# Performance work log

Hardware: AMD Instinct MI355X
Metric: run time of the kernel (lower is better)

Reference implementation:

```python
import jax, jax.numpy as jnp
import numpy as np

N = 65536          # total nodes
B = 64             # graphs in batch
NPG = N // B       # nodes per graph (equal-size graphs)
K = 128            # n_clusters (assignment dim)
D_IN = 128         # node feature dim
D = 128            # pooled feature dim
E = 1048576        # edges (avg degree 16)


def setup_inputs() -> dict:
    key = jax.random.key(0)
    k1, k2, k3, k4, k5, k6 = jax.random.split(key, 6)
    h = jax.random.normal(k1, (N, D_IN), dtype=jnp.float32)
    fea = jax.random.normal(k2, (B * K, D), dtype=jnp.float32)
    W_self = jax.random.normal(k3, (D_IN, K), dtype=jnp.float32) / np.sqrt(D_IN)
    W_neigh = jax.random.normal(k4, (D_IN, K), dtype=jnp.float32) / np.sqrt(D_IN)
    b = jnp.zeros((K,), dtype=jnp.float32)
    # edges kept within each graph: sample local ids then offset by graph base
    base = jnp.repeat(jnp.arange(B, dtype=jnp.int64) * NPG, E // B)
    edge_src = jax.random.randint(k5, (E,), 0, NPG, dtype=jnp.int64) + base
    edge_dst = jax.random.randint(k6, (E,), 0, NPG, dtype=jnp.int64) + base
    return {"h": h, "fea": fea, "W_self": W_self, "W_neigh": W_neigh,
            "b": b, "edge_src": edge_src, "edge_dst": edge_dst}


def reference(h, fea, W_self, W_neigh, b, edge_src, edge_dst):
    # GraphSage mean aggregation: neigh[i] = mean_{j: (j->i)} h[j]
    deg = jnp.zeros((N,), h.dtype).at[edge_dst].add(1.0)
    neigh = jnp.zeros((N, D_IN), h.dtype).at[edge_dst].add(h[edge_src])
    neigh = neigh / jnp.maximum(deg, 1.0)[:, None]
    assign = jax.nn.relu(h @ W_self + neigh @ W_neigh + b)       # [N, K]
    assign = jax.nn.softmax(assign, axis=1)                       # softmax over clusters
    # block-diagonal mm == per-graph GEMM: [B, n, K] @ [B, K, D] -> [B, n, D]
    out = jnp.einsum('bnk,bkd->bnd',
                     assign.reshape(B, NPG, K),
                     fea.reshape(B, K, D))
    return out.reshape(N, D)
```

## Files before the change

### kernel.cpp

```cpp
#include <hip/hip_runtime.h>

#define N_NODES 65536
#define B_G     64
#define NPG     1024
#define KC      128
#define DIN     128
#define E_EDGES 1048576
#define EPG     16384
#define NSLICE  8
#define SLICE_E (EPG / NSLICE)
#define CSTRIDE (EPG + NPG)

typedef __attribute__((ext_vector_type(8))) short short8;
typedef __attribute__((ext_vector_type(4))) float floatx4;

static __device__ __forceinline__ short f2bf(float x) {
    unsigned u = __float_as_uint(x);
    unsigned r = (u + 0x7FFF + ((u >> 16) & 1)) >> 16;
    return (short)r;
}
static __device__ __forceinline__ unsigned pack2(float a, float b) {
    return (unsigned)(unsigned short)f2bf(a) | ((unsigned)(unsigned short)f2bf(b) << 16);
}

__global__ __launch_bounds__(256) void setup_a(
    const float* __restrict__ Wself, const float* __restrict__ Wneigh,
    const float* __restrict__ fea, const float* __restrict__ h,
    const int* __restrict__ edst,
    short* __restrict__ wt, short* __restrict__ feaT, short* __restrict__ h_bf,
    int* __restrict__ slicecnt)
{
    int bid = blockIdx.x;
    int tid = threadIdx.x;
    if (bid < B_G * NSLICE) {
        __shared__ int cnt[NPG];
        int g = bid >> 3, s = bid & 7;
        int gbase = g << 10;
        for (int i = tid; i < NPG; i += 256) cnt[i] = 0;
        __syncthreads();
        const int* ed = edst + (size_t)g * EPG + s * SLICE_E;
#pragma unroll
        for (int it = 0; it < SLICE_E / 256; it++)
            atomicAdd(&cnt[ed[it * 256 + tid] - gbase], 1);
        __syncthreads();
        int* sc = slicecnt + ((size_t)bid << 10);
        for (int i = tid; i < NPG; i += 256) sc[i] = cnt[i];
    } else {
        long idx = (long)(bid - B_G * NSLICE) * 256 + tid;
        if (idx < 32768) {
            int n = (int)(idx >> 8), k = (int)(idx & 255);
            float v = (k < 128) ? Wself[k * 128 + n] : Wneigh[(k - 128) * 128 + n];
            wt[idx] = f2bf(v);
        } else if (idx < 32768 + 1048576) {
            long fi = idx - 32768;
            int g = (int)(fi >> 14), d = (int)((fi >> 7) & 127), k = (int)(fi & 127);
            feaT[fi] = f2bf(fea[((long)g * 128 + k) * 128 + d]);
        } else {
            long gi = idx - 32768 - 1048576;
            const float4* hp = (const float4*)h + gi * 2;
            float4 a = hp[0], b4 = hp[1];
            uint4 w;
            w.x = pack2(a.x, a.y);
            w.y = pack2(a.z, a.w);
            w.z = pack2(b4.x, b4.y);
            w.w = pack2(b4.z, b4.w);
            ((uint4*)h_bf)[gi] = w;
        }
    }
}

__global__ __launch_bounds__(1024) void setup_b(
    const int* __restrict__ slicecnt, int* __restrict__ offs,
    int* __restrict__ deg, int* __restrict__ sliceoffs)
{
    __shared__ int sa[NPG];
    int g = blockIdx.x;
    int tid = threadIdx.x;
    int s8[NSLICE];
    int d = 0;
#pragma unroll
    for (int s = 0; s < NSLICE; s++) {
        s8[s] = slicecnt[(((size_t)g * NSLICE + s) << 10) + tid];
        d += s8[s];
    }
    int p = (d + 1) & ~1;
    sa[tid] = p;
    __syncthreads();
    for (int off = 1; off < NPG; off <<= 1) {
        int v = sa[tid];
        int vv = (tid >= off) ? sa[tid - off] : 0;
        __syncthreads();
        sa[tid] = v + vv;
        __syncthreads();
    }
    int excl = sa[tid] - p;
    offs[(g << 10) + tid] = excl;
    deg[(g << 10) + tid] = d;
    int run = excl;
#pragma unroll
    for (int s = 0; s < NSLICE; s++) {
        sliceoffs[(((size_t)g * NSLICE + s) << 10) + tid] = run;
        run += s8[s];
    }
}

__global__ __launch_bounds__(256) void setup_c(
    const int* __restrict__ esrc, const int* __restrict__ edst,
    const int* __restrict__ sliceoffs, unsigned short* __restrict__ csr)
{
    __shared__ int cur[NPG];
    int bid = blockIdx.x;
    int tid = threadIdx.x;
    int g = bid >> 3, s = bid & 7;
    int gbase = g << 10;
    const int* so = sliceoffs + ((size_t)bid << 10);
    for (int i = tid; i < NPG; i += 256) cur[i] = so[i];
    __syncthreads();
    const int* ed = edst + (size_t)g * EPG + s * SLICE_E;
    const int* es = esrc + (size_t)g * EPG + s * SLICE_E;
    unsigned short* cg = csr + (size_t)g * CSTRIDE;
#pragma unroll
    for (int it = 0; it < SLICE_E / 256; it++) {
        int e = it * 256 + tid;
        int d = ed[e] - gbase;
        int src = es[e] - gbase;
        int pos = atomicAdd(&cur[d], 1);
        cg[pos] = (unsigned short)src;
    }
}

__global__ __launch_bounds__(256) void agg_kernel(
    const short* __restrict__ h_bf, const unsigned short* __restrict__ csr,
    const int* __restrict__ offs, const int* __restrict__ deg,
    short* __restrict__ neigh)
{
    int g = blockIdx.x & 63;
    int chunk = blockIdx.x >> 6;
    int wave = threadIdx.x >> 6, lane = threadIdx.x & 63;
    int local = chunk * 4 + wave;
    int node = g * NPG + local;
    int start = offs[node];
    int m = deg[node];
    const unsigned short* lst = csr + (size_t)g * CSTRIDE + start;
    const uint2* rows = (const uint2*)h_bf + (size_t)g * NPG * 32;
    int l31 = lane & 31;
    int hi = lane >> 5;
    float s0 = 0.f, s1 = 0.f, s2 = 0.f, s3 = 0.f;
    int pairs = m >> 1;
    int p = 0;
    for (; p + 4 <= pairs; p += 4) {
        unsigned pp[4];
#pragma unroll
        for (int u = 0; u < 4; u++) pp[u] = *(const unsigned*)(lst + 2 * (p + u));
        uint2 v[4];
#pragma unroll
        for (int u = 0; u < 4; u++) {
            int s = hi ? (int)(pp[u] >> 16) : (int)(pp[u] & 0xffff);
            v[u] = rows[s * 32 + l31];
        }
#pragma unroll
        for (int u = 0; u < 4; u++) {
            s0 += __uint_as_float(v[u].x << 16);
            s1 += __uint_as_float(v[u].x & 0xffff0000u);
            s2 += __uint_as_float(v[u].y << 16);
            s3 += __uint_as_float(v[u].y & 0xffff0000u);
        }
    }
    for (; p < pairs; p++) {
        unsigned pp = *(const unsigned*)(lst + 2 * p);
        int s = hi ? (int)(pp >> 16) : (int)(pp & 0xffff);
        uint2 vv = rows[s * 32 + l31];
        s0 += __uint_as_float(vv.x << 16);
        s1 += __uint_as_float(vv.x & 0xffff0000u);
        s2 += __uint_as_float(vv.y << 16);
        s3 += __uint_as_float(vv.y & 0xffff0000u);
    }
    if (m & 1) {
        int s = lst[m - 1];
        if (!hi) {
            uint2 vv = rows[s * 32 + l31];
            s0 += __uint_as_float(vv.x << 16);
            s1 += __uint_as_float(vv.x & 0xffff0000u);
            s2 += __uint_as_float(vv.y << 16);
            s3 += __uint_as_float(vv.y & 0xffff0000u);
        }
    }
    s0 += __shfl_xor(s0, 32, 64);
    s1 += __shfl_xor(s1, 32, 64);
    s2 += __shfl_xor(s2, 32, 64);
    s3 += __shfl_xor(s3, 32, 64);
    if (!hi) {
        float invd = 1.0f / fmaxf((float)m, 1.0f);
        uint2 w;
        w.x = pack2(s0 * invd, s1 * invd);
        w.y = pack2(s2 * invd, s3 * invd);
        ((uint2*)neigh)[(size_t)node * 32 + l31] = w;
    }
}

__global__ __launch_bounds__(256) void fused_kernel(
    const short* __restrict__ h_bf, const short* __restrict__ neigh,
    const short* __restrict__ wt, const float* __restrict__ bias,
    const short* __restrict__ feaT, float* __restrict__ out)
{
    __shared__ __align__(16) char smem[50688];
    short* lds_a = (short*)smem;
    short* lds_b = lds_a + 128 * 72;
    short* ldsP  = (short*)smem;
    short* ldsB2 = ldsP + 128 * 132;

    int tid = threadIdx.x;
    int tile_m = blockIdx.x * 128;
    int g = tile_m >> 10;
    int wave = tid >> 6, lane = tid & 63;
    int l15 = lane & 15, quad = lane >> 4;

    floatx4 zz = {0.f, 0.f, 0.f, 0.f};
    floatx4 acc[2][8];
#pragma unroll
    for (int i = 0; i < 2; i++)
#pragma unroll
        for (int j = 0; j < 8; j++) acc[i][j] = zz;

    int row_s = tid >> 1;
    int c0 = (tid & 1) * 32;

    for (int kk = 0; kk < 4; kk++) {
        const short* src = (kk < 2)
            ? h_bf + (size_t)(tile_m + row_s) * DIN + kk * 64 + c0
            : neigh + (size_t)(tile_m + row_s) * DIN + (kk - 2) * 64 + c0;
        short* dsta = lds_a + row_s * 72 + c0;
#pragma unroll
        for (int i = 0; i < 32; i += 8)
            *reinterpret_cast<short8*>(dsta + i) = *reinterpret_cast<const short8*>(src + i);
        const short* srcb = wt + row_s * 256 + kk * 64 + c0;
        short* dstb = lds_b + row_s * 72 + c0;
#pragma unroll
        for (int i = 0; i < 32; i += 8)
            *reinterpret_cast<short8*>(dstb + i) = *reinterpret_cast<const short8*>(srcb + i);
        __syncthreads();
#pragma unroll
        for (int ks = 0; ks < 2; ks++) {
            short8 af[2];
#pragma unroll
            for (int rb = 0; rb < 2; rb++) {
                int m = wave * 32 + rb * 16 + l15;
                af[rb] = *reinterpret_cast<const short8*>(lds_a + m * 72 + ks * 32 + quad * 8);
            }
#pragma unroll
            for (int cb = 0; cb < 8; cb++) {
                int n = cb * 16 + l15;
                short8 bf = *reinterpret_cast<const short8*>(lds_b + n * 72 + ks * 32 + quad * 8);
                acc[0][cb] = __builtin_amdgcn_mfma_f32_16x16x32_bf16(af[0], bf, acc[0][cb], 0, 0, 0);
                acc[1][cb] = __builtin_amdgcn_mfma_f32_16x16x32_bf16(af[1], bf, acc[1][cb], 0, 0, 0);
            }
        }
        __syncthreads();
    }

    float bv[8];
#pragma unroll
    for (int cb = 0; cb < 8; cb++) bv[cb] = bias[cb * 16 + l15];

#pragma unroll
    for (int rb = 0; rb < 2; rb++) {
#pragma unroll
        for (int v = 0; v < 4; v++) {
            float x[8];
            float m = -1e30f;
#pragma unroll
            for (int cb = 0; cb < 8; cb++) {
                float t = acc[rb][cb][v] + bv[cb];
                t = fmaxf(t, 0.f);
                x[cb] = t;
                m = fmaxf(m, t);
            }
#pragma unroll
            for (int off = 1; off < 16; off <<= 1) m = fmaxf(m, __shfl_xor(m, off, 64));
            float s = 0.f;
#pragma unroll
            for (int cb = 0; cb < 8; cb++) { x[cb] = __expf(x[cb] - m); s += x[cb]; }
#pragma unroll
            for (int off = 1; off < 16; off <<= 1) s += __shfl_xor(s, off, 64);
            float inv = 1.0f / s;
            int row = wave * 32 + rb * 16 + quad * 4 + v;
#pragma unroll
            for (int cb = 0; cb < 8; cb++)
                ldsP[row * 132 + cb * 16 + l15] = f2bf(x[cb] * inv);
        }
    }

    floatx4 oacc[2][8];
#pragma unroll
    for (int i = 0; i < 2; i++)
#pragma unroll
        for (int j = 0; j < 8; j++) oacc[i][j] = zz;

    int r2 = tid >> 2;
    int c2 = (tid & 3) * 32;
    short8 pf[2][4];

    for (int half = 0; half < 2; half++) {
        if (half) __syncthreads();
        const short* srcb = feaT + ((size_t)g * 128 + half * 64 + r2) * 128 + c2;
        short* dstb = ldsB2 + r2 * 132 + c2;
#pragma unroll
        for (int i = 0; i < 32; i += 8)
            *reinterpret_cast<short8*>(dstb + i) = *reinterpret_cast<const short8*>(srcb + i);
        __syncthreads();
        if (half == 0) {
#pragma unroll
            for (int rb = 0; rb < 2; rb++)
#pragma unroll
                for (int ks = 0; ks < 4; ks++)
                    pf[rb][ks] = *reinterpret_cast<const short8*>(
                        ldsP + (wave * 32 + rb * 16 + l15) * 132 + ks * 32 + quad * 8);
        }
#pragma unroll
        for (int cb2 = 0; cb2 < 4; cb2++) {
            int cb = half * 4 + cb2;
#pragma unroll
            for (int ks = 0; ks < 4; ks++) {
                short8 bf = *reinterpret_cast<const short8*>(
                    ldsB2 + (cb2 * 16 + l15) * 132 + ks * 32 + quad * 8);
                oacc[0][cb] = __builtin_amdgcn_mfma_f32_16x16x32_bf16(pf[0][ks], bf, oacc[0][cb], 0, 0, 0);
                oacc[1][cb] = __builtin_amdgcn_mfma_f32_16x16x32_bf16(pf[1][ks], bf, oacc[1][cb], 0, 0, 0);
            }
        }
    }

#pragma unroll
    for (int rb = 0; rb < 2; rb++)
#pragma unroll
        for (int v = 0; v < 4; v++) {
            int row = tile_m + wave * 32 + rb * 16 + quad * 4 + v;
#pragma unroll
            for (int cb = 0; cb < 8; cb++)
                out[(size_t)row * 128 + cb * 16 + l15] = oacc[rb][cb][v];
        }
}

extern "C" void kernel_launch(void* const* d_in, const int* in_sizes, int n_in,
                              void* d_out, int out_size, void* d_ws, size_t ws_size,
                              hipStream_t stream) {
    const float* h      = (const float*)d_in[0];
    const float* fea    = (const float*)d_in[1];
    const float* Wself  = (const float*)d_in[2];
    const float* Wneigh = (const float*)d_in[3];
    const float* bias   = (const float*)d_in[4];
    const int*   esrc   = (const int*)d_in[5];
    const int*   edst   = (const int*)d_in[6];
    float* out = (float*)d_out;

    char* ws = (char*)d_ws;
    short* h_bf = (short*)ws;
    size_t off = (size_t)N_NODES * DIN * sizeof(short);
    short* neigh = (short*)(ws + off); off += (size_t)N_NODES * DIN * sizeof(short);
    short* wt    = (short*)(ws + off); off += (size_t)128 * 256 * sizeof(short);
    short* feaT  = (short*)(ws + off); off += (size_t)B_G * 128 * 128 * sizeof(short);
    unsigned short* csr = (unsigned short*)(ws + off); off += (size_t)B_G * CSTRIDE * sizeof(short);
    int* offs = (int*)(ws + off); off += (size_t)N_NODES * sizeof(int);
    int* deg  = (int*)(ws + off); off += (size_t)N_NODES * sizeof(int);
    int* slicecnt  = (int*)(ws + off); off += (size_t)B_G * NSLICE * NPG * sizeof(int);
    int* sliceoffs = (int*)(ws + off);

    setup_a<<<B_G * NSLICE + 8320, 256, 0, stream>>>(Wself, Wneigh, fea, h, edst,
                                                     wt, feaT, h_bf, slicecnt);
    setup_b<<<B_G, 1024, 0, stream>>>(slicecnt, offs, deg, sliceoffs);
    setup_c<<<B_G * NSLICE, 256, 0, stream>>>(esrc, edst, sliceoffs, csr);
    agg_kernel<<<256 * B_G, 256, 0, stream>>>(h_bf, csr, offs, deg, neigh);
    fused_kernel<<<N_NODES / 128, 256, 0, stream>>>(h_bf, neigh, wt, bias, feaT, out);
}
```

Measured before the change: 175.6 us.

## Fuse scan into CSR build and aggregation into GEMM kernel, drop LDS staging

Result: slower. 234.6 us (+33.6%).

```diff
diff --git a/kernel.cpp b/kernel.cpp
--- a/kernel.cpp
+++ b/kernel.cpp
@@ -10,6 +10,7 @@
 #define NSLICE  8
 #define SLICE_E (EPG / NSLICE)
 #define CSTRIDE (EPG + NPG)
+#define NSTR    136
 
 typedef __attribute__((ext_vector_type(8))) short short8;
 typedef __attribute__((ext_vector_type(4))) float floatx4;
@@ -69,52 +70,57 @@
     }
 }
 
-__global__ __launch_bounds__(1024) void setup_b(
-    const int* __restrict__ slicecnt, int* __restrict__ offs,
-    int* __restrict__ deg, int* __restrict__ sliceoffs)
+__global__ __launch_bounds__(256) void setup_sc(
+    const int* __restrict__ esrc, const int* __restrict__ edst,
+    const int* __restrict__ slicecnt, unsigned short* __restrict__ csr,
+    int* __restrict__ offs, int* __restrict__ deg)
 {
-    __shared__ int sa[NPG];
-    int g = blockIdx.x;
-    int tid = threadIdx.x;
-    int s8[NSLICE];
-    int d = 0;
-#pragma unroll
-    for (int s = 0; s < NSLICE; s++) {
-        s8[s] = slicecnt[(((size_t)g * NSLICE + s) << 10) + tid];
-        d += s8[s];
-    }
-    int p = (d + 1) & ~1;
-    sa[tid] = p;
-    __syncthreads();
-    for (int off = 1; off < NPG; off <<= 1) {
-        int v = sa[tid];
-        int vv = (tid >= off) ? sa[tid - off] : 0;
-        __syncthreads();
-        sa[tid] = v + vv;
-        __syncthreads();
-    }
-    int excl = sa[tid] - p;
-    offs[(g << 10) + tid] = excl;
-    deg[(g << 10) + tid] = d;
-    int run = excl;
-#pragma unroll
-    for (int s = 0; s < NSLICE; s++) {
-        sliceoffs[(((size_t)g * NSLICE + s) << 10) + tid] = run;
-        run += s8[s];
-    }
-}
-
-__global__ __launch_bounds__(256) void setup_c(
-    const int* __restrict__ esrc, const int* __restrict__ edst,
-    const int* __restrict__ sliceoffs, unsigned short* __restrict__ csr)
-{
+    __shared__ int ssc[256];
     __shared__ int cur[NPG];
     int bid = blockIdx.x;
-    int tid = threadIdx.x;
     int g = bid >> 3, s = bid & 7;
     int gbase = g << 10;
-    const int* so = sliceoffs + ((size_t)bid << 10);
-    for (int i = tid; i < NPG; i += 256) cur[i] = so[i];
+    int tid = threadIdx.x;
+    int scv[NSLICE][4];
+#pragma unroll
+    for (int sl = 0; sl < NSLICE; sl++) {
+        const int* sc = slicecnt + (((size_t)g * NSLICE + sl) << 10);
+#pragma unroll
+        for (int i = 0; i < 4; i++) scv[sl][i] = sc[4 * tid + i];
+    }
+    int d[4], p[4], lsum = 0;
+#pragma unroll
+    for (int i = 0; i < 4; i++) {
+        d[i] = 0;
+#pragma unroll
+        for (int sl = 0; sl < NSLICE; sl++) d[i] += scv[sl][i];
+        p[i] = (d[i] + 1) & ~1;
+        lsum += p[i];
+    }
+    ssc[tid] = lsum;
+    __syncthreads();
+    for (int off = 1; off < 256; off <<= 1) {
+        int v = ssc[tid];
+        int vv = (tid >= off) ? ssc[tid - off] : 0;
+        __syncthreads();
+        ssc[tid] = v + vv;
+        __syncthreads();
+    }
+    int base = ssc[tid] - lsum;
+#pragma unroll
+    for (int i = 0; i < 4; i++) {
+        int node = 4 * tid + i;
+        if (s == 0) {
+            offs[gbase + node] = base;
+            deg[gbase + node] = d[i];
+        }
+        int c = base;
+#pragma unroll
+        for (int sl = 0; sl < NSLICE; sl++)
+            if (sl < s) c += scv[sl][i];
+        cur[node] = c;
+        base += p[i];
+    }
     __syncthreads();
     const int* ed = edst + (size_t)g * EPG + s * SLICE_E;
     const int* es = esrc + (size_t)g * EPG + s * SLICE_E;
@@ -122,98 +128,89 @@
 #pragma unroll
     for (int it = 0; it < SLICE_E / 256; it++) {
         int e = it * 256 + tid;
-        int d = ed[e] - gbase;
-        int src = es[e] - gbase;
-        int pos = atomicAdd(&cur[d], 1);
-        cg[pos] = (unsigned short)src;
-    }
-}
-
-__global__ __launch_bounds__(256) void agg_kernel(
+        int dd = ed[e] - gbase;
+        int sv = es[e] - gbase;
+        int pos = atomicAdd(&cur[dd], 1);
+        cg[pos] = (unsigned short)sv;
+    }
+}
+
+__global__ __launch_bounds__(256) void fused_all(
     const short* __restrict__ h_bf, const unsigned short* __restrict__ csr,
-    const int* __restrict__ offs, const int* __restrict__ deg,
-    short* __restrict__ neigh)
+    const int* __restrict__ offs, const int* __restrict__ deg_,
+    const short* __restrict__ wt, const float* __restrict__ bias,
+    const short* __restrict__ feaT, float* __restrict__ out)
 {
-    int g = blockIdx.x & 63;
-    int chunk = blockIdx.x >> 6;
-    int wave = threadIdx.x >> 6, lane = threadIdx.x & 63;
-    int local = chunk * 4 + wave;
-    int node = g * NPG + local;
-    int start = offs[node];
-    int m = deg[node];
-    const unsigned short* lst = csr + (size_t)g * CSTRIDE + start;
-    const uint2* rows = (const uint2*)h_bf + (size_t)g * NPG * 32;
-    int l31 = lane & 31;
-    int hi = lane >> 5;
-    float s0 = 0.f, s1 = 0.f, s2 = 0.f, s3 = 0.f;
-    int pairs = m >> 1;
-    int p = 0;
-    for (; p + 4 <= pairs; p += 4) {
-        unsigned pp[4];
-#pragma unroll
-        for (int u = 0; u < 4; u++) pp[u] = *(const unsigned*)(lst + 2 * (p + u));
-        uint2 v[4];
-#pragma unroll
-        for (int u = 0; u < 4; u++) {
-            int s = hi ? (int)(pp[u] >> 16) : (int)(pp[u] & 0xffff);
-            v[u] = rows[s * 32 + l31];
-        }
-#pragma unroll
-        for (int u = 0; u < 4; u++) {
-            s0 += __uint_as_float(v[u].x << 16);
-            s1 += __uint_as_float(v[u].x & 0xffff0000u);
-            s2 += __uint_as_float(v[u].y << 16);
-            s3 += __uint_as_float(v[u].y & 0xffff0000u);
-        }
-    }
-    for (; p < pairs; p++) {
-        unsigned pp = *(const unsigned*)(lst + 2 * p);
-        int s = hi ? (int)(pp >> 16) : (int)(pp & 0xffff);
-        uint2 vv = rows[s * 32 + l31];
-        s0 += __uint_as_float(vv.x << 16);
-        s1 += __uint_as_float(vv.x & 0xffff0000u);
-        s2 += __uint_as_float(vv.y << 16);
-        s3 += __uint_as_float(vv.y & 0xffff0000u);
-    }
-    if (m & 1) {
-        int s = lst[m - 1];
-        if (!hi) {
+    __shared__ __align__(16) short ldsN[128 * NSTR];
+
+    int tid = threadIdx.x;
+    int tile = blockIdx.x;
+    int g = tile >> 3;
+    int tile_m = tile * 128;
+    int wave = tid >> 6, lane = tid & 63;
+    int l31 = lane & 31, hi = lane >> 5;
+    int l15 = lane & 15, quad = lane >> 4;
+
+    const uint2* rows = (const uint2*)h_bf + ((size_t)g << 10) * 32;
+    const unsigned short* cbase = csr + (size_t)g * CSTRIDE;
+    for (int t = 0; t < 32; t++) {
+        int node = tile_m + wave * 32 + t;
+        int start = offs[node];
+        int m = deg_[node];
+        const unsigned short* lst = cbase + start;
+        float s0 = 0.f, s1 = 0.f, s2 = 0.f, s3 = 0.f;
+        int pairs = m >> 1;
+        int p = 0;
+        for (; p + 4 <= pairs; p += 4) {
+            unsigned pp[4];
+#pragma unroll
+            for (int u = 0; u < 4; u++) pp[u] = *(const unsigned*)(lst + 2 * (p + u));
+            uint2 v[4];
+#pragma unroll
+            for (int u = 0; u < 4; u++) {
+                int s = hi ? (int)(pp[u] >> 16) : (int)(pp[u] & 0xffff);
+                v[u] = rows[s * 32 + l31];
+            }
+#pragma unroll
+            for (int u = 0; u < 4; u++) {
+                s0 += __uint_as_float(v[u].x << 16);
+                s1 += __uint_as_float(v[u].x & 0xffff0000u);
+                s2 += __uint_as_float(v[u].y << 16);
+                s3 += __uint_as_float(v[u].y & 0xffff0000u);
+            }
+        }
+        for (; p < pairs; p++) {
+            unsigned pp = *(const unsigned*)(lst + 2 * p);
+            int s = hi ? (int)(pp >> 16) : (int)(pp & 0xffff);
             uint2 vv = rows[s * 32 + l31];
             s0 += __uint_as_float(vv.x << 16);
             s1 += __uint_as_float(vv.x & 0xffff0000u);
             s2 += __uint_as_float(vv.y << 16);
             s3 += __uint_as_float(vv.y & 0xffff0000u);
         }
-    }
-    s0 += __shfl_xor(s0, 32, 64);
-    s1 += __shfl_xor(s1, 32, 64);
-    s2 += __shfl_xor(s2, 32, 64);
-    s3 += __shfl_xor(s3, 32, 64);
-    if (!hi) {
-        float invd = 1.0f / fmaxf((float)m, 1.0f);
-        uint2 w;
-        w.x = pack2(s0 * invd, s1 * invd);
-        w.y = pack2(s2 * invd, s3 * invd);
-        ((uint2*)neigh)[(size_t)node * 32 + l31] = w;
-    }
-}
-
-__global__ __launch_bounds__(256) void fused_kernel(
-    const short* __restrict__ h_bf, const short* __restrict__ neigh,
-    const short* __restrict__ wt, const float* __restrict__ bias,
-    const short* __restrict__ feaT, float* __restrict__ out)
-{
-    __shared__ __align__(16) char smem[50688];
-    short* lds_a = (short*)smem;
-    short* lds_b = lds_a + 128 * 72;
-    short* ldsP  = (short*)smem;
-    short* ldsB2 = ldsP + 128 * 132;
-
-    int tid = threadIdx.x;
-    int tile_m = blockIdx.x * 128;
-    int g = tile_m >> 10;
-    int wave = tid >> 6, lane = tid & 63;
-    int l15 = lane & 15, quad = lane >> 4;
+        if (m & 1) {
+            int s = lst[m - 1];
+            if (!hi) {
+                uint2 vv = rows[s * 32 + l31];
+                s0 += __uint_as_float(vv.x << 16);
+                s1 += __uint_as_float(vv.x & 0xffff0000u);
+                s2 += __uint_as_float(vv.y << 16);
+                s3 += __uint_as_float(vv.y & 0xffff0000u);
+            }
+        }
+        s0 += __shfl_xor(s0, 32, 64);
+        s1 += __shfl_xor(s1, 32, 64);
+        s2 += __shfl_xor(s2, 32, 64);
+        s3 += __shfl_xor(s3, 32, 64);
+        if (!hi) {
+            float invd = 1.0f / fmaxf((float)m, 1.0f);
+            uint2 w;
+            w.x = pack2(s0 * invd, s1 * invd);
+            w.y = pack2(s2 * invd, s3 * invd);
+            *(uint2*)(ldsN + (wave * 32 + t) * NSTR + l31 * 4) = w;
+        }
+    }
+    __syncthreads();
 
     floatx4 zz = {0.f, 0.f, 0.f, 0.f};
     floatx4 acc[2][8];
@@ -222,40 +219,29 @@
 #pragma unroll
         for (int j = 0; j < 8; j++) acc[i][j] = zz;
 
-    int row_s = tid >> 1;
-    int c0 = (tid & 1) * 32;
-
+#pragma unroll
     for (int kk = 0; kk < 4; kk++) {
-        const short* src = (kk < 2)
-            ? h_bf + (size_t)(tile_m + row_s) * DIN + kk * 64 + c0
-            : neigh + (size_t)(tile_m + row_s) * DIN + (kk - 2) * 64 + c0;
-        short* dsta = lds_a + row_s * 72 + c0;
-#pragma unroll
-        for (int i = 0; i < 32; i += 8)
-            *reinterpret_cast<short8*>(dsta + i) = *reinterpret_cast<const short8*>(src + i);
-        const short* srcb = wt + row_s * 256 + kk * 64 + c0;
-        short* dstb = lds_b + row_s * 72 + c0;
-#pragma unroll
-        for (int i = 0; i < 32; i += 8)
-            *reinterpret_cast<short8*>(dstb + i) = *reinterpret_cast<const short8*>(srcb + i);
-        __syncthreads();
 #pragma unroll
         for (int ks = 0; ks < 2; ks++) {
             short8 af[2];
 #pragma unroll
             for (int rb = 0; rb < 2; rb++) {
                 int m = wave * 32 + rb * 16 + l15;
-                af[rb] = *reinterpret_cast<const short8*>(lds_a + m * 72 + ks * 32 + quad * 8);
+                if (kk < 2)
+                    af[rb] = *reinterpret_cast<const short8*>(
+                        h_bf + (size_t)(tile_m + m) * DIN + kk * 64 + ks * 32 + quad * 8);
+                else
+                    af[rb] = *reinterpret_cast<const short8*>(
+                        ldsN + m * NSTR + (kk - 2) * 64 + ks * 32 + quad * 8);
             }
 #pragma unroll
             for (int cb = 0; cb < 8; cb++) {
-                int n = cb * 16 + l15;
-                short8 bf = *reinterpret_cast<const short8*>(lds_b + n * 72 + ks * 32 + quad * 8);
+                short8 bf = *reinterpret_cast<const short8*>(
+                    wt + (cb * 16 + l15) * 256 + kk * 64 + ks * 32 + quad * 8);
                 acc[0][cb] = __builtin_amdgcn_mfma_f32_16x16x32_bf16(af[0], bf, acc[0][cb], 0, 0, 0);
                 acc[1][cb] = __builtin_amdgcn_mfma_f32_16x16x32_bf16(af[1], bf, acc[1][cb], 0, 0, 0);
             }
         }
-        __syncthreads();
     }
 
     float bv[8];
@@ -286,9 +272,10 @@
             int row = wave * 32 + rb * 16 + quad * 4 + v;
 #pragma unroll
             for (int cb = 0; cb < 8; cb++)
-                ldsP[row * 132 + cb * 16 + l15] = f2bf(x[cb] * inv);
-        }
-    }
+                ldsN[row * NSTR + cb * 16 + l15] = f2bf(x[cb] * inv);
+        }
+    }
+    __syncthreads();
 
     floatx4 oacc[2][8];
 #pragma unroll
@@ -296,36 +283,22 @@
 #pragma unroll
         for (int j = 0; j < 8; j++) oacc[i][j] = zz;
 
-    int r2 = tid >> 2;
-    int c2 = (tid & 3) * 32;
     short8 pf[2][4];
-
-    for (int half = 0; half < 2; half++) {
-        if (half) __syncthreads();
-        const short* srcb = feaT + ((size_t)g * 128 + half * 64 + r2) * 128 + c2;
-        short* dstb = ldsB2 + r2 * 132 + c2;
-#pragma unroll
-        for (int i = 0; i < 32; i += 8)
-            *reinterpret_cast<short8*>(dstb + i) = *reinterpret_cast<const short8*>(srcb + i);
-        __syncthreads();
-        if (half == 0) {
-#pragma unroll
-            for (int rb = 0; rb < 2; rb++)
-#pragma unroll
-                for (int ks = 0; ks < 4; ks++)
-                    pf[rb][ks] = *reinterpret_cast<const short8*>(
-                        ldsP + (wave * 32 + rb * 16 + l15) * 132 + ks * 32 + quad * 8);
-        }
-#pragma unroll
-        for (int cb2 = 0; cb2 < 4; cb2++) {
-            int cb = half * 4 + cb2;
-#pragma unroll
-            for (int ks = 0; ks < 4; ks++) {
-                short8 bf = *reinterpret_cast<const short8*>(
-                    ldsB2 + (cb2 * 16 + l15) * 132 + ks * 32 + quad * 8);
-                oacc[0][cb] = __builtin_amdgcn_mfma_f32_16x16x32_bf16(pf[0][ks], bf, oacc[0][cb], 0, 0, 0);
-                oacc[1][cb] = __builtin_amdgcn_mfma_f32_16x16x32_bf16(pf[1][ks], bf, oacc[1][cb], 0, 0, 0);
-            }
+#pragma unroll
+    for (int rb = 0; rb < 2; rb++)
+#pragma unroll
+        for (int ks = 0; ks < 4; ks++)
+            pf[rb][ks] = *reinterpret_cast<const short8*>(
+                ldsN + (wave * 32 + rb * 16 + l15) * NSTR + ks * 32 + quad * 8);
+
+#pragma unroll
+    for (int cb = 0; cb < 8; cb++) {
+#pragma unroll
+        for (int ks = 0; ks < 4; ks++) {
+            short8 bf = *reinterpret_cast<const short8*>(
+                feaT + ((size_t)(g * 128) + cb * 16 + l15) * 128 + ks * 32 + quad * 8);
+            oacc[0][cb] = __builtin_amdgcn_mfma_f32_16x16x32_bf16(pf[0][ks], bf, oacc[0][cb], 0, 0, 0);
+            oacc[1][cb] = __builtin_amdgcn_mfma_f32_16x16x32_bf16(pf[1][ks], bf, oacc[1][cb], 0, 0, 0);
         }
     }
 
@@ -355,19 +328,15 @@
     char* ws = (char*)d_ws;
     short* h_bf = (short*)ws;
     size_t off = (size_t)N_NODES * DIN * sizeof(short);
-    short* neigh = (short*)(ws + off); off += (size_t)N_NODES * DIN * sizeof(short);
     short* wt    = (short*)(ws + off); off += (size_t)128 * 256 * sizeof(short);
     short* feaT  = (short*)(ws + off); off += (size_t)B_G * 128 * 128 * sizeof(short);
     unsigned short* csr = (unsigned short*)(ws + off); off += (size_t)B_G * CSTRIDE * sizeof(short);
     int* offs = (int*)(ws + off); off += (size_t)N_NODES * sizeof(int);
     int* deg  = (int*)(ws + off); off += (size_t)N_NODES * sizeof(int);
-    int* slicecnt  = (int*)(ws + off); off += (size_t)B_G * NSLICE * NPG * sizeof(int);
-    int* sliceoffs = (int*)(ws + off);
+    int* slicecnt = (int*)(ws + off);
 
     setup_a<<<B_G * NSLICE + 8320, 256, 0, stream>>>(Wself, Wneigh, fea, h, edst,
                                                      wt, feaT, h_bf, slicecnt);
-    setup_b<<<B_G, 1024, 0, stream>>>(slicecnt, offs, deg, sliceoffs);
-    setup_c<<<B_G * NSLICE, 256, 0, stream>>>(esrc, edst, sliceoffs, csr);
-    agg_kernel<<<256 * B_G, 256, 0, stream>>>(h_bf, csr, offs, deg, neigh);
-    fused_kernel<<<N_NODES / 128, 256, 0, stream>>>(h_bf, neigh, wt, bias, feaT, out);
-}
+    setup_sc<<<B_G * NSLICE, 256, 0, stream>>>(esrc, edst, slicecnt, csr, offs, deg);
+    fused_all<<<N_NODES / 128, 256, 0, stream>>>(h_bf, csr, offs, deg, wt, bias, feaT, out);
+}
```
